# Kernel tuning notes

Measured on AMD Instinct MI355X. Metric: run time of the kernel, lower is better.

## Reference

```python
import jax, jax.numpy as jnp
import numpy as np

N = 100000      # nodes
E = 1600000     # edges (before self loops)
IN_C, HID_C, OUT_C = 128, 64, 40


def setup_inputs() -> dict:
    key = jax.random.key(0)
    k = jax.random.split(key, 6)
    x = jax.random.normal(k[0], (N, IN_C), dtype=jnp.float32)
    edge_index = jax.random.randint(k[1], (2, E), 0, N, dtype=jnp.int64)
    W1 = jax.random.normal(k[2], (IN_C, HID_C), dtype=jnp.float32) * (1.0 / np.sqrt(IN_C))
    b1 = jnp.zeros((HID_C,), jnp.float32)
    W2 = jax.random.normal(k[3], (HID_C, OUT_C), dtype=jnp.float32) * (1.0 / np.sqrt(HID_C))
    b2 = jnp.zeros((OUT_C,), jnp.float32)
    beta2 = jnp.ones((), jnp.float32)  # learnable beta of prop2 (init 1.0)
    return {"x": x, "edge_index": edge_index, "W1": W1, "b1": b1,
            "W2": W2, "b2": b2, "beta2": beta2}


def _agnn_prop(x, src, dst, beta, n):
    # L2-normalize node features (F.normalize, eps=1e-12 on norm)
    xn = x * jax.lax.rsqrt(jnp.maximum(jnp.sum(x * x, axis=-1, keepdims=True), 1e-24))
    # per-edge cosine similarity scaled by beta
    alpha = beta * jnp.sum(xn[src] * xn[dst], axis=-1)           # [E']
    # scatter-softmax over edges grouped by destination node
    amax = jax.ops.segment_max(alpha, dst, num_segments=n)       # [N]
    e = jnp.exp(alpha - amax[dst])
    denom = jax.ops.segment_sum(e, dst, num_segments=n)          # [N]
    w = e / denom[dst]                                           # [E']
    # gather-weighted aggregation of (unnormalized) source features
    return jax.ops.segment_sum(x[src] * w[:, None], dst, num_segments=n)


def reference(x, edge_index, W1, b1, W2, b2, beta2):
    n = x.shape[0]
    # AGNNConv add_self_loops=True
    loops = jnp.arange(n, dtype=edge_index.dtype)
    src = jnp.concatenate([edge_index[0], loops])
    dst = jnp.concatenate([edge_index[1], loops])
    h = jax.nn.relu(x @ W1 + b1)                                 # [N, HID]
    h = _agnn_prop(h, src, dst, jnp.float32(1.0), n)             # prop1: fixed beta=1
    h = _agnn_prop(h, src, dst, beta2, n)                        # prop2: learnable beta
    logits = h @ W2 + b2                                         # [N, OUT]
    return jax.nn.log_softmax(logits, axis=1)
```

## Files before the change

### kernel.cpp

```cpp
#include <hip/hip_runtime.h>
#include <math.h>

#define INC 128
#define HID 64
#define OUTC 40
#define SHIFT 9
#define MAXB 256
#define NPB 64
#define ONB 96
#define LSW 41

typedef _Float16 half2_t __attribute__((ext_vector_type(2)));

__device__ inline void fma4(float4& a, float s, const float4& w) {
    a.x += s * w.x; a.y += s * w.y; a.z += s * w.z; a.w += s * w.w;
}
__device__ inline unsigned pkh(float a, float b) {
    unsigned short ua = __builtin_bit_cast(unsigned short, (_Float16)a);
    unsigned short ub = __builtin_bit_cast(unsigned short, (_Float16)b);
    return (unsigned)ua | ((unsigned)ub << 16);
}
__device__ inline float fdot2_(unsigned a, unsigned b, float c) {
#if __has_builtin(__builtin_amdgcn_fdot2)
    return __builtin_amdgcn_fdot2(__builtin_bit_cast(half2_t, a),
                                  __builtin_bit_cast(half2_t, b), c, false);
#else
    half2_t ha = __builtin_bit_cast(half2_t, a);
    half2_t hb = __builtin_bit_cast(half2_t, b);
    return fmaf((float)ha[0], (float)hb[0], fmaf((float)ha[1], (float)hb[1], c));
#endif
}
__device__ inline float dot4(const uint4& a, const uint4& b) {
    float d = fdot2_(a.x, b.x, 0.f);
    d = fdot2_(a.y, b.y, d);
    d = fdot2_(a.z, b.z, d);
    d = fdot2_(a.w, b.w, d);
    return d;
}
__device__ inline void accum8(float* acc, float s, const uint4& a) {
    half2_t p;
    p = __builtin_bit_cast(half2_t, a.x); acc[0] += s * (float)p[0]; acc[1] += s * (float)p[1];
    p = __builtin_bit_cast(half2_t, a.y); acc[2] += s * (float)p[0]; acc[3] += s * (float)p[1];
    p = __builtin_bit_cast(half2_t, a.z); acc[4] += s * (float)p[0]; acc[5] += s * (float)p[1];
    p = __builtin_bit_cast(half2_t, a.w); acc[6] += s * (float)p[0]; acc[7] += s * (float)p[1];
}
__device__ inline void unpack8(float* f, const uint4& a) {
    half2_t p;
    p = __builtin_bit_cast(half2_t, a.x); f[0] = (float)p[0]; f[1] = (float)p[1];
    p = __builtin_bit_cast(half2_t, a.y); f[2] = (float)p[0]; f[3] = (float)p[1];
    p = __builtin_bit_cast(half2_t, a.z); f[4] = (float)p[0]; f[5] = (float)p[1];
    p = __builtin_bit_cast(half2_t, a.w); f[6] = (float)p[0]; f[7] = (float)p[1];
}
__device__ inline void dacc4(float4& a, unsigned xp_, const uint4& w) {
    a.x = fdot2_(xp_, w.x, a.x);
    a.y = fdot2_(xp_, w.y, a.y);
    a.z = fdot2_(xp_, w.z, a.z);
    a.w = fdot2_(xp_, w.w, a.w);
}
#define EXP2(x) __builtin_amdgcn_exp2f(x)


__global__ __launch_bounds__(256) void k_hist(const int* __restrict__ ei, int E,
                                              int* __restrict__ bucket_cnt,
                                              int* __restrict__ blk_cnt, int nbuck) {
    __shared__ int lh[MAXB];
    int tid = threadIdx.x;
    for (int i = tid; i < nbuck; i += 256) lh[i] = 0;
    __syncthreads();
    int base = blockIdx.x * 4096;
    int end = min(base + 4096, E);
    for (int e = base + tid; e < end; e += 256)
        atomicAdd(&lh[ei[E + e] >> SHIFT], 1);
    __syncthreads();
    for (int i = tid; i < nbuck; i += 256) {
        int v = lh[i];
        blk_cnt[blockIdx.x * MAXB + i] = v;
        if (v) atomicAdd(&bucket_cnt[i], v);
    }
}

__global__ __launch_bounds__(256) void k_bscan(const int* __restrict__ bucket_cnt,
                                               int* __restrict__ pair_base,
                                               int* __restrict__ pair_fill,
                                               int* __restrict__ row_ptr,
                                               int n, int E, int nbuck) {
    __shared__ int tmp[MAXB];
    int tid = threadIdx.x;
    int cnt = (tid < nbuck) ? bucket_cnt[tid] : 0;
    tmp[tid] = cnt;
    __syncthreads();
    for (int off = 1; off < 256; off <<= 1) {
        int t = (tid >= off) ? tmp[tid - off] : 0;
        __syncthreads();
        tmp[tid] += t;
        __syncthreads();
    }
    if (tid < nbuck) { int pb = tmp[tid] - cnt; pair_base[tid] = pb; pair_fill[tid] = pb; }
    if (tid == 0) row_ptr[n] = E;
}

__global__ __launch_bounds__(256) void k_bin(const int* __restrict__ ei, int E,
                                             const int* __restrict__ blk_cnt,
                                             int* __restrict__ pair_fill,
                                             int2* __restrict__ pairs, int nbuck) {
    __shared__ int lbase[MAXB];
    int tid = threadIdx.x;
    for (int i = tid; i < nbuck; i += 256) {
        int v = blk_cnt[blockIdx.x * MAXB + i];
        lbase[i] = v ? atomicAdd(&pair_fill[i], v) : 0;
    }
    __syncthreads();
    int base = blockIdx.x * 4096;
    int end = min(base + 4096, E);
    for (int e = base + tid; e < end; e += 256) {
        int s = ei[e], d = ei[E + e];
        int pos = atomicAdd(&lbase[d >> SHIFT], 1);
        pairs[pos] = make_int2(s, d);
    }
}

__global__ __launch_bounds__(256) void k_build(const int2* __restrict__ pairs,
                                               const int* __restrict__ pair_base,
                                               const int* __restrict__ bucket_cnt,
                                               int* __restrict__ row_ptr,
                                               int* __restrict__ csr_src, int n) {
    __shared__ int cnt[1 << SHIFT];
    __shared__ int offs[1 << SHIFT];
    __shared__ int stmp[256];
    int b = blockIdx.x;
    int tid = threadIdx.x;
    int nb0 = b << SHIFT;
    int W = min(n - nb0, 1 << SHIFT);
    int p0 = pair_base[b], pc = bucket_cnt[b];

    cnt[tid] = 0; cnt[tid + 256] = 0;
    __syncthreads();
    for (int i = tid; i < pc; i += 256)
        atomicAdd(&cnt[pairs[p0 + i].y - nb0], 1);
    __syncthreads();

    int i0 = 2 * tid, i1 = 2 * tid + 1;
    int s0 = (i0 < W) ? cnt[i0] : 0;
    int s1 = (i1 < W) ? cnt[i1] : 0;
    int ps = s0 + s1;
    stmp[tid] = ps;
    __syncthreads();
    for (int off = 1; off < 256; off <<= 1) {
        int t = (tid >= off) ? stmp[tid - off] : 0;
        __syncthreads();
        stmp[tid] += t;
        __syncthreads();
    }
    int excl = stmp[tid] - ps;
    if (i0 < W) { row_ptr[nb0 + i0] = p0 + excl;      offs[i0] = excl; }
    if (i1 < W) { row_ptr[nb0 + i1] = p0 + excl + s0; offs[i1] = excl + s0; }
    __syncthreads();
    for (int i = tid; i < pc; i += 256) {
        int2 pr = pairs[p0 + i];
        int pos = atomicAdd(&offs[pr.y - nb0], 1);
        csr_src[p0 + pos] = pr.x;
    }
}


__global__ __launch_bounds__(256, 4) void k_linear1(const float* __restrict__ x,
                                                    const float* __restrict__ W1,
                                                    const float* __restrict__ b1,
                                                    uint2* __restrict__ X1,
                                                    float* __restrict__ nrm1, int n) {
    __shared__ unsigned Wp[64 * 64];
    __shared__ unsigned xp[64 * 64];
    int tid = threadIdx.x;
    int base = blockIdx.x * NPB;

    for (int t = tid; t < 1024; t += 256) {
        int kp = t >> 4;
        int c4 = t & 15;
        float4 a = ((const float4*)W1)[(2 * kp) * 16 + c4];
        float4 b = ((const float4*)W1)[(2 * kp + 1) * 16 + c4];
        uint4 w;
        w.x = pkh(a.x, b.x); w.y = pkh(a.y, b.y);
        w.z = pkh(a.z, b.z); w.w = pkh(a.w, b.w);
        *(uint4*)&Wp[kp * 64 + c4 * 4] = w;
    }
    for (int t = tid; t < 1024; t += 256) {
        int nl = t >> 4;
        int k8 = t & 15;
        int gn = base + nl;
        float4 a, b;
        if (gn < n) {
            a = ((const float4*)x)[(size_t)gn * 32 + k8 * 2];
            b = ((const float4*)x)[(size_t)gn * 32 + k8 * 2 + 1];
        } else { a = make_float4(0,0,0,0); b = a; }
        uint4 v;
        v.x = pkh(a.x, a.y); v.y = pkh(a.z, a.w);
        v.z = pkh(b.x, b.y); v.w = pkh(b.z, b.w);
        int key = ((nl >> 2) & 3) << 2;
        *(uint4*)&xp[nl * 64 + ((k8 * 4) ^ key)] = v;
    }
    __syncthreads();

    int cg = tid & 15;
    int ng = tid >> 4;
    int n0 = ng * 4;
    const int key = (ng & 3) << 2;
    float4 acc0 = {0,0,0,0}, acc1 = {0,0,0,0}, acc2 = {0,0,0,0}, acc3 = {0,0,0,0};

    #pragma unroll 4
    for (int k4 = 0; k4 < 64; k4 += 4) {
        uint4 xq0 = *(uint4*)&xp[(n0 + 0) * 64 + (k4 ^ key)];
        uint4 xq1 = *(uint4*)&xp[(n0 + 1) * 64 + (k4 ^ key)];
        uint4 xq2 = *(uint4*)&xp[(n0 + 2) * 64 + (k4 ^ key)];
        uint4 xq3 = *(uint4*)&xp[(n0 + 3) * 64 + (k4 ^ key)];
        uint4 wq0 = *(uint4*)&Wp[(k4 + 0) * 64 + cg * 4];
        uint4 wq1 = *(uint4*)&Wp[(k4 + 1) * 64 + cg * 4];
        uint4 wq2 = *(uint4*)&Wp[(k4 + 2) * 64 + cg * 4];
        uint4 wq3 = *(uint4*)&Wp[(k4 + 3) * 64 + cg * 4];
        dacc4(acc0, xq0.x, wq0); dacc4(acc0, xq0.y, wq1); dacc4(acc0, xq0.z, wq2); dacc4(acc0, xq0.w, wq3);
        dacc4(acc1, xq1.x, wq0); dacc4(acc1, xq1.y, wq1); dacc4(acc1, xq1.z, wq2); dacc4(acc1, xq1.w, wq3);
        dacc4(acc2, xq2.x, wq0); dacc4(acc2, xq2.y, wq1); dacc4(acc2, xq2.z, wq2); dacc4(acc2, xq2.w, wq3);
        dacc4(acc3, xq3.x, wq0); dacc4(acc3, xq3.y, wq1); dacc4(acc3, xq3.z, wq2); dacc4(acc3, xq3.w, wq3);
    }

    float4 bb = ((const float4*)b1)[cg];
    float4 r[4] = {acc0, acc1, acc2, acc3};
    #pragma unroll
    for (int nl = 0; nl < 4; ++nl) {
        int node = base + n0 + nl;
        float4 v = r[nl];
        v.x = fmaxf(v.x + bb.x, 0.f); v.y = fmaxf(v.y + bb.y, 0.f);
        v.z = fmaxf(v.z + bb.z, 0.f); v.w = fmaxf(v.w + bb.w, 0.f);
        float q = v.x * v.x + v.y * v.y + v.z * v.z + v.w * v.w;
        #pragma unroll
        for (int off = 8; off >= 1; off >>= 1) q += __shfl_xor(q, off, 64);
        float rq = rsqrtf(fmaxf(q, 1e-24f));
        if (node < n) {
            X1[(size_t)node * 16 + cg] = make_uint2(pkh(v.x * rq, v.y * rq),
                                                    pkh(v.z * rq, v.w * rq));
            if (cg == 0) nrm1[node] = sqrtf(fmaxf(q, 1e-24f));
        }
    }
}


template<bool HFOUT>
__global__ __launch_bounds__(256) void k_prop(const uint4* __restrict__ X,
                                              const float* __restrict__ nrm,
                                              const int* __restrict__ row_ptr,
                                              const int* __restrict__ csr_src,
                                              const float* __restrict__ beta_ptr,
                                              uint4* __restrict__ Xout,
                                              float* __restrict__ nrm_out,
                                              float4* __restrict__ outf, int n) {
    int node = blockIdx.x * 4 + (threadIdx.x >> 6);
    if (node >= n) return;
    int lane = threadIdx.x & 63;
    int g = lane >> 3, gl = lane & 7;
    float beta = beta_ptr ? beta_ptr[0] : 1.0f;
    float b2 = beta * 1.4426950408889634f;

    uint4 hdp = X[(size_t)node * 8 + gl];
    float hdf[8]; unpack8(hdf, hdp);
    int s0 = row_ptr[node], s1 = row_ptr[node + 1];

    float ds = dot4(hdp, hdp);
    ds += __shfl_xor(ds, 1, 64); ds += __shfl_xor(ds, 2, 64); ds += __shfl_xor(ds, 4, 64);
    float eself = EXP2(b2 * ds);
    float nd = nrm[node];
    float den0 = (g == 0) ? eself : 0.f;
    float es = (g == 0) ? eself * nd : 0.f;
    float acc[8];
    #pragma unroll
    for (int c = 0; c < 8; ++c) acc[c] = es * hdf[c];
    float den1 = 0.f;

    for (int j = s0; j < s1; j += 16) {
        int p0 = j + g, p1 = j + 8 + g;
        bool v0 = p0 < s1, v1 = p1 < s1;
        int i0 = v0 ? csr_src[p0] : 0;
        int i1 = v1 ? csr_src[p1] : 0;
        uint4 a0 = X[(size_t)i0 * 8 + gl];
        uint4 a1 = X[(size_t)i1 * 8 + gl];
        float n0 = nrm[i0], n1 = nrm[i1];
        float d0 = dot4(a0, hdp);
        float d1 = dot4(a1, hdp);
        d0 += __shfl_xor(d0, 1, 64); d1 += __shfl_xor(d1, 1, 64);
        d0 += __shfl_xor(d0, 2, 64); d1 += __shfl_xor(d1, 2, 64);
        d0 += __shfl_xor(d0, 4, 64); d1 += __shfl_xor(d1, 4, 64);
        float e0 = v0 ? EXP2(b2 * d0) : 0.f;
        float e1 = v1 ? EXP2(b2 * d1) : 0.f;
        den0 += e0; den1 += e1;
        float sc0 = e0 * n0, sc1 = e1 * n1;
        accum8(acc, sc0, a0);
        accum8(acc, sc1, a1);
    }

    float den = den0 + den1;
    #pragma unroll
    for (int c = 0; c < 8; ++c) {
        acc[c] += __shfl_xor(acc[c], 8, 64);
        acc[c] += __shfl_xor(acc[c], 16, 64);
        acc[c] += __shfl_xor(acc[c], 32, 64);
    }
    den += __shfl_xor(den, 8, 64);
    den += __shfl_xor(den, 16, 64);
    den += __shfl_xor(den, 32, 64);
    float inv = 1.0f / den;
    float o[8];
    #pragma unroll
    for (int c = 0; c < 8; ++c) o[c] = acc[c] * inv;

    if (HFOUT) {
        float q = 0.f;
        #pragma unroll
        for (int c = 0; c < 8; ++c) q += o[c] * o[c];
        q += __shfl_xor(q, 1, 64); q += __shfl_xor(q, 2, 64); q += __shfl_xor(q, 4, 64);
        float rq = rsqrtf(fmaxf(q, 1e-24f));
        if (g == 0) {
            uint4 w;
            w.x = pkh(o[0] * rq, o[1] * rq);
            w.y = pkh(o[2] * rq, o[3] * rq);
            w.z = pkh(o[4] * rq, o[5] * rq);
            w.w = pkh(o[6] * rq, o[7] * rq);
            Xout[(size_t)node * 8 + gl] = w;
            if (gl == 0) nrm_out[node] = sqrtf(fmaxf(q, 1e-24f));
        }
    } else {
        if (g == 0) {
            outf[(size_t)node * 16 + gl * 2]     = make_float4(o[0], o[1], o[2], o[3]);
            outf[(size_t)node * 16 + gl * 2 + 1] = make_float4(o[4], o[5], o[6], o[7]);
        }
    }
}


__global__ __launch_bounds__(256) void k_out(const float* __restrict__ h,
                                             const float* __restrict__ W2,
                                             const float* __restrict__ b2,
                                             float* __restrict__ out, int n) {
    __shared__ float hs[ONB * HID];
    __shared__ float W2s[HID * OUTC];
    __shared__ float ls[ONB * LSW];
    int tid = threadIdx.x;
    int base = blockIdx.x * ONB;

    for (int i = tid; i < HID * OUTC / 4; i += 256)
        ((float4*)W2s)[i] = ((const float4*)W2)[i];
    for (int i = tid; i < ONB * 16; i += 256) {
        int nl = i >> 4, k4 = i & 15;
        int gn = base + nl;
        float4 v = (gn < n) ? ((const float4*)h)[(size_t)gn * 16 + k4]
                            : make_float4(0.f, 0.f, 0.f, 0.f);
        int swk = (k4 * 4) ^ (((nl >> 2) & 7) << 2);
        *(float4*)&hs[nl * HID + swk] = v;
    }
    __syncthreads();

    if (tid < 240) {
        int ng = tid / 10, cg = tid % 10;
        int n0 = ng * 4;
        const int sw = ((ng & 7) << 2);
        float4 acc0 = {0,0,0,0}, acc1 = {0,0,0,0}, acc2 = {0,0,0,0}, acc3 = {0,0,0,0};
        #pragma unroll 4
        for (int k = 0; k < HID; k += 4) {
            float4 w0 = *(float4*)&W2s[(k + 0) * OUTC + cg * 4];
            float4 w1 = *(float4*)&W2s[(k + 1) * OUTC + cg * 4];
            float4 w2 = *(float4*)&W2s[(k + 2) * OUTC + cg * 4];
            float4 w3 = *(float4*)&W2s[(k + 3) * OUTC + cg * 4];
            float4 x0 = *(float4*)&hs[(n0 + 0) * HID + (k ^ sw)];
            float4 x1 = *(float4*)&hs[(n0 + 1) * HID + (k ^ sw)];
            float4 x2 = *(float4*)&hs[(n0 + 2) * HID + (k ^ sw)];
            float4 x3 = *(float4*)&hs[(n0 + 3) * HID + (k ^ sw)];
            fma4(acc0, x0.x, w0); fma4(acc0, x0.y, w1); fma4(acc0, x0.z, w2); fma4(acc0, x0.w, w3);
            fma4(acc1, x1.x, w0); fma4(acc1, x1.y, w1); fma4(acc1, x1.z, w2); fma4(acc1, x1.w, w3);
            fma4(acc2, x2.x, w0); fma4(acc2, x2.y, w1); fma4(acc2, x2.z, w2); fma4(acc2, x2.w, w3);
            fma4(acc3, x3.x, w0); fma4(acc3, x3.y, w1); fma4(acc3, x3.z, w2); fma4(acc3, x3.w, w3);
        }
        float4 bb = ((const float4*)b2)[cg];
        float4 rr[4] = {acc0, acc1, acc2, acc3};
        #pragma unroll
        for (int i = 0; i < 4; ++i) {
            int lb = (n0 + i) * LSW + cg * 4;
            ls[lb + 0] = rr[i].x + bb.x;
            ls[lb + 1] = rr[i].y + bb.y;
            ls[lb + 2] = rr[i].z + bb.z;
            ls[lb + 3] = rr[i].w + bb.w;
        }
    }
    __syncthreads();

    if (tid < ONB) {
        int node = base + tid;
        if (node < n) {
            float m = -INFINITY;
            #pragma unroll
            for (int c = 0; c < OUTC; ++c) m = fmaxf(m, ls[tid * LSW + c]);
            float z = 0.f;
            #pragma unroll
            for (int c = 0; c < OUTC; ++c) z += __expf(ls[tid * LSW + c] - m);
            float lz = m + __logf(z);
            #pragma unroll
            for (int c = 0; c < OUTC; ++c)
                out[(size_t)node * OUTC + c] = ls[tid * LSW + c] - lz;
        }
    }
}


extern "C" void kernel_launch(void* const* d_in, const int* in_sizes, int n_in,
                              void* d_out, int out_size, void* d_ws, size_t ws_size,
                              hipStream_t stream) {
    const float* x   = (const float*)d_in[0];
    const int*   ei  = (const int*)d_in[1];
    const float* W1  = (const float*)d_in[2];
    const float* b1  = (const float*)d_in[3];
    const float* W2  = (const float*)d_in[4];
    const float* b2  = (const float*)d_in[5];
    const float* beta2 = (const float*)d_in[6];
    float* out = (float*)d_out;

    const int n = in_sizes[0] / INC;
    const int E = in_sizes[1] / 2;
    const int nbuck = (n + (1 << SHIFT) - 1) >> SHIFT;
    const int cgrid = (E + 4095) / 4096;

    char* p = (char*)d_ws;
    uint4* X1 = (uint4*)p;             p += (size_t)n * 8 * 16;
    uint4* X2 = (uint4*)p;             p += (size_t)n * 8 * 16;
    float* h3 = (float*)p;             p += (size_t)n * HID * 4;
    float* nrm1 = (float*)p;           p += (size_t)n * 4;
    float* nrm2 = (float*)p;           p += (size_t)n * 4;
    int* bucket_cnt  = (int*)p;        p += MAXB * 4;
    int* pair_base   = (int*)p;        p += MAXB * 4;
    int* pair_fill   = (int*)p;        p += MAXB * 4;
    int* row_ptr = (int*)p;            p += (size_t)(n + 1) * 4;
    int* csr_src = (int*)p;            p += (size_t)E * 4;
    int* blk_cnt = (int*)p;            p += (size_t)cgrid * MAXB * 4;
    int2* pairs = (int2*)h3;

    hipMemsetAsync(bucket_cnt, 0, MAXB * 4, stream);
    k_hist<<<cgrid, 256, 0, stream>>>(ei, E, bucket_cnt, blk_cnt, nbuck);
    k_bscan<<<1, 256, 0, stream>>>(bucket_cnt, pair_base, pair_fill, row_ptr, n, E, nbuck);
    k_bin<<<cgrid, 256, 0, stream>>>(ei, E, blk_cnt, pair_fill, pairs, nbuck);
    k_build<<<nbuck, 256, 0, stream>>>(pairs, pair_base, bucket_cnt, row_ptr, csr_src, n);

    k_linear1<<<(n + NPB - 1) / NPB, 256, 0, stream>>>(x, W1, b1, (uint2*)X1, nrm1, n);
    int pgrid = (n + 3) / 4;
    k_prop<true><<<pgrid, 256, 0, stream>>>(X1, nrm1, row_ptr, csr_src, nullptr,
                                            X2, nrm2, nullptr, n);
    k_prop<false><<<pgrid, 256, 0, stream>>>(X2, nrm2, row_ptr, csr_src, beta2,
                                             nullptr, nullptr, (float4*)h3, n);
    k_out<<<(n + ONB - 1) / ONB, 256, 0, stream>>>(h3, W2, b2, out, n);
}
```

Baseline: 220.1 us.

## Pack CSR build pairs into 32 bits and use DPP reductions in prop

The binning stage now stores each edge as one 32-bit word: a 17-bit source index plus the destination's offset within its bucket, instead of an int2. This halves the scratch traffic written in k_bin and read twice in k_build. Separately, the butterfly shuffle reductions over 8 and 16 lanes in linear1 and prop are replaced with DPP row operations, which avoid LDS-based cross-lane traffic. The packing assumes node indices fit in 17 bits, which holds for N=100000 but would break for larger graphs.

```diff
diff --git a/kernel.cpp b/kernel.cpp
--- a/kernel.cpp
+++ b/kernel.cpp
@@ -9,6 +9,7 @@
 #define NPB 64
 #define ONB 96
 #define LSW 41
+#define SRCM 0x1FFFF
 
 typedef _Float16 half2_t __attribute__((ext_vector_type(2)));
 
@@ -57,6 +58,25 @@
     a.z = fdot2_(xp_, w.z, a.z);
     a.w = fdot2_(xp_, w.w, a.w);
 }
+template<int CTRL>
+__device__ inline float dppadd(float d) {
+    int x = __builtin_amdgcn_update_dpp(0, __builtin_bit_cast(int, d),
+                                        CTRL, 0xf, 0xf, true);
+    return d + __builtin_bit_cast(float, x);
+}
+__device__ inline float red8(float d) {
+    d = dppadd<0xB1>(d);
+    d = dppadd<0x4E>(d);
+    d = dppadd<0x141>(d);
+    return d;
+}
+__device__ inline float red16(float d) {
+    d = dppadd<0xB1>(d);
+    d = dppadd<0x4E>(d);
+    d = dppadd<0x141>(d);
+    d = dppadd<0x140>(d);
+    return d;
+}
 #define EXP2(x) __builtin_amdgcn_exp2f(x)
 
 
@@ -102,7 +122,7 @@
 __global__ __launch_bounds__(256) void k_bin(const int* __restrict__ ei, int E,
                                              const int* __restrict__ blk_cnt,
                                              int* __restrict__ pair_fill,
-                                             int2* __restrict__ pairs, int nbuck) {
+                                             unsigned* __restrict__ pairs, int nbuck) {
     __shared__ int lbase[MAXB];
     int tid = threadIdx.x;
     for (int i = tid; i < nbuck; i += 256) {
@@ -115,11 +135,11 @@
     for (int e = base + tid; e < end; e += 256) {
         int s = ei[e], d = ei[E + e];
         int pos = atomicAdd(&lbase[d >> SHIFT], 1);
-        pairs[pos] = make_int2(s, d);
-    }
-}
-
-__global__ __launch_bounds__(256) void k_build(const int2* __restrict__ pairs,
+        pairs[pos] = (unsigned)s | ((unsigned)(d & ((1 << SHIFT) - 1)) << 17);
+    }
+}
+
+__global__ __launch_bounds__(256) void k_build(const unsigned* __restrict__ pairs,
                                                const int* __restrict__ pair_base,
                                                const int* __restrict__ bucket_cnt,
                                                int* __restrict__ row_ptr,
@@ -136,7 +156,7 @@
     cnt[tid] = 0; cnt[tid + 256] = 0;
     __syncthreads();
     for (int i = tid; i < pc; i += 256)
-        atomicAdd(&cnt[pairs[p0 + i].y - nb0], 1);
+        atomicAdd(&cnt[pairs[p0 + i] >> 17], 1);
     __syncthreads();
 
     int i0 = 2 * tid, i1 = 2 * tid + 1;
@@ -156,9 +176,9 @@
     if (i1 < W) { row_ptr[nb0 + i1] = p0 + excl + s0; offs[i1] = excl + s0; }
     __syncthreads();
     for (int i = tid; i < pc; i += 256) {
-        int2 pr = pairs[p0 + i];
-        int pos = atomicAdd(&offs[pr.y - nb0], 1);
-        csr_src[p0 + pos] = pr.x;
+        unsigned pr = pairs[p0 + i];
+        int pos = atomicAdd(&offs[pr >> 17], 1);
+        csr_src[p0 + pos] = (int)(pr & SRCM);
     }
 }
 
@@ -231,8 +251,7 @@
         v.x = fmaxf(v.x + bb.x, 0.f); v.y = fmaxf(v.y + bb.y, 0.f);
         v.z = fmaxf(v.z + bb.z, 0.f); v.w = fmaxf(v.w + bb.w, 0.f);
         float q = v.x * v.x + v.y * v.y + v.z * v.z + v.w * v.w;
-        #pragma unroll
-        for (int off = 8; off >= 1; off >>= 1) q += __shfl_xor(q, off, 64);
+        q = red16(q);
         float rq = rsqrtf(fmaxf(q, 1e-24f));
         if (node < n) {
             X1[(size_t)node * 16 + cg] = make_uint2(pkh(v.x * rq, v.y * rq),
@@ -263,8 +282,7 @@
     float hdf[8]; unpack8(hdf, hdp);
     int s0 = row_ptr[node], s1 = row_ptr[node + 1];
 
-    float ds = dot4(hdp, hdp);
-    ds += __shfl_xor(ds, 1, 64); ds += __shfl_xor(ds, 2, 64); ds += __shfl_xor(ds, 4, 64);
+    float ds = red8(dot4(hdp, hdp));
     float eself = EXP2(b2 * ds);
     float nd = nrm[node];
     float den0 = (g == 0) ? eself : 0.f;
@@ -282,11 +300,8 @@
         uint4 a0 = X[(size_t)i0 * 8 + gl];
         uint4 a1 = X[(size_t)i1 * 8 + gl];
         float n0 = nrm[i0], n1 = nrm[i1];
-        float d0 = dot4(a0, hdp);
-        float d1 = dot4(a1, hdp);
-        d0 += __shfl_xor(d0, 1, 64); d1 += __shfl_xor(d1, 1, 64);
-        d0 += __shfl_xor(d0, 2, 64); d1 += __shfl_xor(d1, 2, 64);
-        d0 += __shfl_xor(d0, 4, 64); d1 += __shfl_xor(d1, 4, 64);
+        float d0 = red8(dot4(a0, hdp));
+        float d1 = red8(dot4(a1, hdp));
         float e0 = v0 ? EXP2(b2 * d0) : 0.f;
         float e1 = v1 ? EXP2(b2 * d1) : 0.f;
         den0 += e0; den1 += e1;
@@ -314,7 +329,7 @@
         float q = 0.f;
         #pragma unroll
         for (int c = 0; c < 8; ++c) q += o[c] * o[c];
-        q += __shfl_xor(q, 1, 64); q += __shfl_xor(q, 2, 64); q += __shfl_xor(q, 4, 64);
+        q = red8(q);
         float rq = rsqrtf(fmaxf(q, 1e-24f));
         if (g == 0) {
             uint4 w;
@@ -436,7 +451,7 @@
     int* row_ptr = (int*)p;            p += (size_t)(n + 1) * 4;
     int* csr_src = (int*)p;            p += (size_t)E * 4;
     int* blk_cnt = (int*)p;            p += (size_t)cgrid * MAXB * 4;
-    int2* pairs = (int2*)h3;
+    unsigned* pairs = (unsigned*)h3;
 
     hipMemsetAsync(bucket_cnt, 0, MAXB * 4, stream);
     k_hist<<<cgrid, 256, 0, stream>>>(ei, E, bucket_cnt, blk_cnt, nbuck);
```

New measurement: 206.6 us. -6.1%, faster.
